# Kernel optimization log

Hardware: AMD Instinct MI355X
Metric: run time of the kernel (lower is better)

The kernel has to match this reference:

```python
import jax, jax.numpy as jnp
import numpy as np

N_HEADS = 8
D_MODEL = 512
D_HEAD = 64
INIT_RANGE = 0.02
B = 2
T = 192
IGNORE = -1000000.0


def setup_inputs() -> dict:
    key = jax.random.key(0)
    ks = jax.random.split(key, 10)
    def p(k, shape):
        return jax.random.normal(k, shape, dtype=jnp.float32) * INIT_RANGE
    inp = {
        "normalized_resid_pre": jax.random.normal(ks[0], (B, T, D_MODEL), dtype=jnp.float32),
        "W_A": p(ks[1], (N_HEADS, D_MODEL, D_HEAD)),
        "W_B": p(ks[2], (N_HEADS, D_MODEL, D_HEAD)),
        "W_C": p(ks[3], (N_HEADS, D_MODEL, D_HEAD)),
        "W_D": p(ks[4], (N_HEADS, D_MODEL, D_HEAD)),
        "W_E": p(ks[5], (N_HEADS, D_MODEL, D_HEAD)),
        "W_K": p(ks[6], (N_HEADS, D_HEAD, D_HEAD, D_HEAD)),
        "W_V": p(ks[7], (N_HEADS, D_HEAD, D_HEAD, D_HEAD)),
        "W_O": p(ks[8], (N_HEADS, D_HEAD, D_MODEL)),
        "b_A": jnp.zeros((N_HEADS, D_HEAD), jnp.float32),
        "b_B": jnp.zeros((N_HEADS, D_HEAD), jnp.float32),
        "b_C": jnp.zeros((N_HEADS, D_HEAD), jnp.float32),
        "b_D": jnp.zeros((N_HEADS, D_HEAD), jnp.float32),
        "b_E": jnp.zeros((N_HEADS, D_HEAD), jnp.float32),
        "b_O": jnp.zeros((D_MODEL,), jnp.float32),
    }
    return inp


def reference(normalized_resid_pre, W_A, W_B, W_C, W_D, W_E, W_K, W_V, W_O,
              b_A, b_B, b_C, b_D, b_E, b_O):
    x = normalized_resid_pre
    bs, ts, _ = x.shape
    # Per-head linear projections: [b, p, n, h]
    a = jnp.einsum('ndh,bpd->bpnh', W_A, x) + b_A
    b = jnp.einsum('ndh,bpd->bpnh', W_B, x) + b_B
    c = jnp.einsum('ndh,bpd->bpnh', W_C, x) + b_C
    d = jnp.einsum('ndh,bpd->bpnh', W_D, x) + b_D
    e = jnp.einsum('ndh,bpd->bpnh', W_E, x) + b_E
    # Pairwise value tensor: v[b, p1, p2, n, h3]
    v = jnp.einsum('bpnh,bqng,nhgk->bpqnk', d, e, W_V)
    # Cubic key contraction. NOTE: step2 sums over heads of b (faithful to original einsum).
    step1 = jnp.einsum('brnk,nijk->brij', c, W_K)        # [b, p3, i, j]
    step2 = jnp.einsum('brij,bqnj->briq', step1, b)      # [b, p3, i, p2]
    scores = jnp.einsum('briq,bpni->bnpqr', step2, a)    # [b, n, p1, p2, p3]
    # Causal mask (order_attn=True): mask where p1 >= p2 or p1 >= p3
    i1 = jnp.arange(ts)[:, None, None]
    i2 = jnp.arange(ts)[None, :, None]
    i3 = jnp.arange(ts)[None, None, :]
    mask = (i1 >= i2) | (i1 >= i3)
    scores = jnp.where(mask, IGNORE, scores)
    # [b, n, p3, p1*p2], scaled by d_head
    scores = scores.transpose(0, 1, 4, 2, 3).reshape(bs, N_HEADS, ts, ts * ts) / D_HEAD
    extra = jnp.full((bs, N_HEADS, ts, 1), -1000.0, scores.dtype)
    probs = jax.nn.softmax(jnp.concatenate([scores, extra], axis=-1), axis=-1)
    # v -> [b, n, h, p1*p2], append zero slot matching the extra score column
    vflat = v.transpose(0, 3, 4, 1, 2).reshape(bs, N_HEADS, D_HEAD, ts * ts)
    vflat = jnp.concatenate([vflat, jnp.zeros((bs, N_HEADS, D_HEAD, 1), vflat.dtype)], axis=-1)
    z = jnp.einsum('bnql,bnhl->bqnh', probs, vflat)
    out = jnp.einsum('bpnh,nhd->bpd', z, W_O) + b_O
    return out
```

## Files before the change

### kernel.cpp

```cpp
#include <hip/hip_runtime.h>
#include <hip/hip_bf16.h>
#include <math.h>


#define OFF_A      0u
#define OFF_Bp     196608u
#define OFF_C      393216u
#define OFF_D      589824u
#define OFF_E      786432u
#define OFF_BSUM   983040u
#define OFF_S1     1007616u
#define OFF_S2     2580480u
#define OFF_Z      7299072u

typedef short s8v __attribute__((ext_vector_type(8)));
typedef float f4v __attribute__((ext_vector_type(4)));

static __device__ __forceinline__ unsigned short f2bf(float f) {
  union { float f; unsigned int u; } v; v.f = f;
  unsigned int r = v.u + 0x7FFFu + ((v.u >> 16) & 1u);
  return (unsigned short)(r >> 16);
}


__device__ __forceinline__ void load_At(const float* __restrict__ Aptr, int lda,
                                        float* __restrict__ As, int t) {
  int r = t >> 2, c4 = (t & 3) * 4;
  const float4 v = *(const float4*)(Aptr + r * lda + c4);
  As[(c4 + 0) * 68 + r] = v.x;
  As[(c4 + 1) * 68 + r] = v.y;
  As[(c4 + 2) * 68 + r] = v.z;
  As[(c4 + 3) * 68 + r] = v.w;
}

__device__ __forceinline__ void mm_acc16(const float* __restrict__ As,
                                         const float* __restrict__ Bs,
                                         float acc[4][4], int tm4, int tn4) {
#pragma unroll
  for (int kk = 0; kk < 16; ++kk) {
    const float4 a = *(const float4*)(As + kk * 68 + tm4);
    const float4 b = *(const float4*)(Bs + kk * 68 + tn4);
    acc[0][0] += a.x * b.x; acc[0][1] += a.x * b.y; acc[0][2] += a.x * b.z; acc[0][3] += a.x * b.w;
    acc[1][0] += a.y * b.x; acc[1][1] += a.y * b.y; acc[1][2] += a.y * b.z; acc[1][3] += a.y * b.w;
    acc[2][0] += a.z * b.x; acc[2][1] += a.z * b.y; acc[2][2] += a.z * b.z; acc[2][3] += a.z * b.w;
    acc[3][0] += a.w * b.x; acc[3][1] += a.w * b.y; acc[3][2] += a.w * b.z; acc[3][3] += a.w * b.w;
  }
}


__global__ void k_proj(const float* __restrict__ x,
                       const float* __restrict__ W0, const float* __restrict__ W1,
                       const float* __restrict__ W2, const float* __restrict__ W3,
                       const float* __restrict__ W4,
                       const float* __restrict__ bi0, const float* __restrict__ bi1,
                       const float* __restrict__ bi2, const float* __restrict__ bi3,
                       const float* __restrict__ bi4,
                       float* __restrict__ ws) {
  const int wsel = blockIdx.z;
  const float* W = wsel == 0 ? W0 : wsel == 1 ? W1 : wsel == 2 ? W2 : wsel == 3 ? W3 : W4;
  const float* bias = wsel == 0 ? bi0 : wsel == 1 ? bi1 : wsel == 2 ? bi2 : wsel == 3 ? bi3 : bi4;
  float* out = ws + (size_t)wsel * 196608u;

  const int m0 = blockIdx.x * 64;
  const int c0 = blockIdx.y * 64;
  const int nblk = c0 >> 6;
  __shared__ float As[16 * 68], Bs[16 * 68];
  const int t = threadIdx.x;
  const int tm4 = (t >> 4) * 4, tn4 = (t & 15) * 4;
  float acc[4][4] = {};

  for (int k0 = 0; k0 < 512; k0 += 16) {
    load_At(x + m0 * 512 + k0, 512, As, t);
#pragma unroll
    for (int it = 0; it < 4; ++it) {
      int kk = (t >> 6) + it * 4, cc = t & 63;
      Bs[kk * 68 + cc] = W[nblk * 32768 + (k0 + kk) * 64 + cc];
    }
    __syncthreads();
    mm_acc16(As, Bs, acc, tm4, tn4);
    __syncthreads();
  }
  const float4 bv = *(const float4*)&bias[c0 + tn4];
#pragma unroll
  for (int i = 0; i < 4; ++i) {
    float4 v;
    v.x = acc[i][0] + bv.x; v.y = acc[i][1] + bv.y; v.z = acc[i][2] + bv.z; v.w = acc[i][3] + bv.w;
    *(float4*)&out[(m0 + tm4 + i) * 512 + c0 + tn4] = v;
  }
}


__global__ void k_bsum(const float* __restrict__ bp, float* __restrict__ out) {
  int idx = blockIdx.x * 256 + threadIdx.x;
  if (idx < 24576) {
    int bq = idx >> 6, j = idx & 63;
    float s = 0.f;
#pragma unroll
    for (int n = 0; n < 8; ++n) s += bp[bq * 512 + n * 64 + j];
    out[idx] = s;
  }
}


__global__ void k_step1(const float* __restrict__ Cp, const float* __restrict__ WK,
                        float* __restrict__ S1) {
  const int m0 = blockIdx.x * 64, c0 = blockIdx.y * 64;
  __shared__ float As[16 * 68], Bs[16 * 68];
  const int t = threadIdx.x;
  const int tm4 = (t >> 4) * 4, tn4 = (t & 15) * 4;
  float acc[4][4] = {};
  for (int k0 = 0; k0 < 512; k0 += 16) {
    load_At(Cp + m0 * 512 + k0, 512, As, t);
#pragma unroll
    for (int it = 0; it < 4; ++it) {
      int kk = t & 15, cc = (t >> 4) + it * 16;
      int k = k0 + kk;
      Bs[kk * 68 + cc] = WK[(k >> 6) * 262144 + (c0 + cc) * 64 + (k & 63)];
    }
    __syncthreads();
    mm_acc16(As, Bs, acc, tm4, tn4);
    __syncthreads();
  }
#pragma unroll
  for (int i = 0; i < 4; ++i) {
    float4 v; v.x = acc[i][0]; v.y = acc[i][1]; v.z = acc[i][2]; v.w = acc[i][3];
    *(float4*)&S1[(size_t)(m0 + tm4 + i) * 4096 + c0 + tn4] = v;
  }
}


__global__ void k_step2(const float* __restrict__ S1, const float* __restrict__ BS,
                        float* __restrict__ S2) {
  const int b = blockIdx.z;
  const int m0 = blockIdx.x * 64, c0 = blockIdx.y * 64;
  const float* A = S1 + (size_t)b * 786432u;
  const float* Bb = BS + b * 12288;
  float* C = S2 + (size_t)b * 2359296u;
  __shared__ float As[16 * 68], Bs[16 * 68];
  const int t = threadIdx.x;
  const int tm4 = (t >> 4) * 4, tn4 = (t & 15) * 4;
  float acc[4][4] = {};
  for (int k0 = 0; k0 < 64; k0 += 16) {
    load_At(A + m0 * 64 + k0, 64, As, t);
#pragma unroll
    for (int it = 0; it < 4; ++it) {
      int kk = t & 15, cc = (t >> 4) + it * 16;
      Bs[kk * 68 + cc] = Bb[(c0 + cc) * 64 + k0 + kk];
    }
    __syncthreads();
    mm_acc16(As, Bs, acc, tm4, tn4);
    __syncthreads();
  }
#pragma unroll
  for (int i = 0; i < 4; ++i) {
    float4 v; v.x = acc[i][0]; v.y = acc[i][1]; v.z = acc[i][2]; v.w = acc[i][3];
    *(float4*)&C[(size_t)(m0 + tm4 + i) * 192 + c0 + tn4] = v;
  }
}

#define X_ST2T 0u
#define X_ET   27648u
#define X_E    53248u
#define X_AS   78848u
#define X_DT   88064u
#define X_FT   97280u
#define X_RED  106496u
#define X_TOT  108544u
#define X_US   0u
#define X_RZ   27648u

extern "C" __global__ void __launch_bounds__(512, 1)
k_attn(const float* __restrict__ st2, const float* __restrict__ eproj,
       const float* __restrict__ aproj, const float* __restrict__ dproj,
       const float* __restrict__ WV, float* __restrict__ zout) {
  extern __shared__ char smc[];
  unsigned short* lus = (unsigned short*)smc;
  float* lf = (float*)smc;
  const int bn = blockIdx.x;
  const int r = 191 - (int)blockIdx.y;
  const int b = bn >> 3, n = bn & 7;
  const int t = threadIdx.x;
  const int lane = t & 63, w = t >> 6;
  const int l15 = lane & 15, kg = lane >> 4;

  const float* st2g = st2 + (size_t)b * 2359296u + (size_t)r * 12288u;
  const float* eg = eproj + (size_t)b * 98304u + n * 64;
  const float* ag = aproj + (size_t)b * 98304u + n * 64;
  const float* dg = dproj + (size_t)b * 98304u + n * 64;

  for (int idx = t; idx < 12288; idx += 512) {
    int i = idx / 192, q = idx - i * 192;
    lus[(X_ST2T >> 1) + q * 72 + i] = f2bf(st2g[idx]);
  }
  for (int idx = t; idx < 12288; idx += 512) {
    int q = idx >> 6, g = idx & 63;
    lus[(X_ET >> 1) + g * 200 + q] = f2bf(eg[q * 512 + g]);
  }

  float Dpart = 0.f;
  f4v U0 = {0.f, 0.f, 0.f, 0.f};
  f4v U1 = {0.f, 0.f, 0.f, 0.f};
  const int ptiles = (r + 63) >> 6;

  for (int pt_i = 0; pt_i < ptiles; ++pt_i) {
    const int p0 = pt_i << 6;
    for (int idx = t; idx < 4096; idx += 512) {
      int p = idx >> 6, c = idx & 63;
      float av = ag[(p0 + p) * 512 + c];
      float dv = dg[(p0 + p) * 512 + c];
      lus[(X_AS >> 1) + p * 72 + c] = f2bf(av);
      lus[(X_DT >> 1) + c * 72 + p] = f2bf(dv);
    }
    __syncthreads();

#pragma unroll
    for (int s = 0; s < 6; ++s) {
      const int tid = w + 8 * s, qt = tid >> 2, pt = tid & 3;
      f4v acc = {0.f, 0.f, 0.f, 0.f};
#pragma unroll
      for (int kb = 0; kb < 2; ++kb) {
        const s8v A = *(const s8v*)&lus[(X_ST2T >> 1) + (qt * 16 + l15) * 72 + kb * 32 + kg * 8];
        const s8v Bf = *(const s8v*)&lus[(X_AS >> 1) + (pt * 16 + l15) * 72 + kb * 32 + kg * 8];
        acc = __builtin_amdgcn_mfma_f32_16x16x32_bf16(A, Bf, acc, 0, 0, 0);
      }
      const int p_loc = pt * 16 + l15, p = p0 + p_loc;
      short4 pk;
      {
        float Ev0 = 0.f, Ev1 = 0.f, Ev2 = 0.f, Ev3 = 0.f;
        const int q0 = qt * 16 + kg * 4;
        if (p < r) {
          if (q0 + 0 > p) { Ev0 = __expf(acc[0] * 0.015625f); Dpart += Ev0; }
          if (q0 + 1 > p) { Ev1 = __expf(acc[1] * 0.015625f); Dpart += Ev1; }
          if (q0 + 2 > p) { Ev2 = __expf(acc[2] * 0.015625f); Dpart += Ev2; }
          if (q0 + 3 > p) { Ev3 = __expf(acc[3] * 0.015625f); Dpart += Ev3; }
        }
        pk.x = (short)f2bf(Ev0); pk.y = (short)f2bf(Ev1);
        pk.z = (short)f2bf(Ev2); pk.w = (short)f2bf(Ev3);
      }
      *(short4*)&lus[(X_E >> 1) + p_loc * 200 + qt * 16 + kg * 4] = pk;
    }
    __syncthreads();

#pragma unroll
    for (int s = 0; s < 2; ++s) {
      const int tid = w + 8 * s, mt = tid >> 2, nt = tid & 3;
      f4v acc = {0.f, 0.f, 0.f, 0.f};
#pragma unroll
      for (int kb = 0; kb < 6; ++kb) {
        const s8v A = *(const s8v*)&lus[(X_E >> 1) + (mt * 16 + l15) * 200 + kb * 32 + kg * 8];
        const s8v Bf = *(const s8v*)&lus[(X_ET >> 1) + (nt * 16 + l15) * 200 + kb * 32 + kg * 8];
        acc = __builtin_amdgcn_mfma_f32_16x16x32_bf16(A, Bf, acc, 0, 0, 0);
      }
      short4 pk;
      pk.x = (short)f2bf(acc[0]); pk.y = (short)f2bf(acc[1]);
      pk.z = (short)f2bf(acc[2]); pk.w = (short)f2bf(acc[3]);
      *(short4*)&lus[(X_FT >> 1) + (nt * 16 + l15) * 72 + mt * 16 + kg * 4] = pk;
    }
    __syncthreads();

    {
      const int tid0 = w, ht0 = tid0 >> 2, gt0 = tid0 & 3;
#pragma unroll
      for (int kb = 0; kb < 2; ++kb) {
        const s8v A = *(const s8v*)&lus[(X_DT >> 1) + (ht0 * 16 + l15) * 72 + kb * 32 + kg * 8];
        const s8v Bf = *(const s8v*)&lus[(X_FT >> 1) + (gt0 * 16 + l15) * 72 + kb * 32 + kg * 8];
        U0 = __builtin_amdgcn_mfma_f32_16x16x32_bf16(A, Bf, U0, 0, 0, 0);
      }
      const int tid1 = w + 8, ht1 = tid1 >> 2, gt1 = tid1 & 3;
#pragma unroll
      for (int kb = 0; kb < 2; ++kb) {
        const s8v A = *(const s8v*)&lus[(X_DT >> 1) + (ht1 * 16 + l15) * 72 + kb * 32 + kg * 8];
        const s8v Bf = *(const s8v*)&lus[(X_FT >> 1) + (gt1 * 16 + l15) * 72 + kb * 32 + kg * 8];
        U1 = __builtin_amdgcn_mfma_f32_16x16x32_bf16(A, Bf, U1, 0, 0, 0);
      }
    }
    __syncthreads();
  }

  lf[(X_RED >> 2) + t] = Dpart;
  __syncthreads();
  for (int off = 256; off > 0; off >>= 1) {
    if (t < off) lf[(X_RED >> 2) + t] += lf[(X_RED >> 2) + t + off];
    __syncthreads();
  }
  const float Dfull = lf[X_RED >> 2];
  const float invD = Dfull > 0.f ? 1.f / Dfull : 0.f;
  __syncthreads();

  {
    const int ht0 = w >> 2, gt0 = w & 3;
#pragma unroll
    for (int j = 0; j < 4; ++j)
      lf[(X_US >> 2) + (gt0 * 16 + l15) * 66 + ht0 * 16 + kg * 4 + j] = U0[j] * invD;
    const int ht1 = (w + 8) >> 2, gt1 = (w + 8) & 3;
#pragma unroll
    for (int j = 0; j < 4; ++j)
      lf[(X_US >> 2) + (gt1 * 16 + l15) * 66 + ht1 * 16 + kg * 4 + j] = U1[j] * invD;
  }
  __syncthreads();

  const float* WVn = WV + (size_t)n * 262144u;
  const int k4 = (t & 15) * 4, hh = t >> 4;
  float zx = 0.f, zy = 0.f, zz = 0.f, zw = 0.f;
#pragma unroll
  for (int hi = 0; hi < 2; ++hi) {
    const int h = hh * 2 + hi;
    const float* wr = WVn + (size_t)h * 4096 + k4;
    for (int g = 0; g < 64; ++g) {
      const float u = lf[(X_US >> 2) + g * 66 + h];
      const float4 wv = *(const float4*)(wr + g * 64);
      zx += u * wv.x; zy += u * wv.y; zz += u * wv.z; zw += u * wv.w;
    }
  }
  { float4 zp; zp.x = zx; zp.y = zy; zp.z = zz; zp.w = zw;
    *(float4*)&lf[(X_RZ >> 2) + hh * 64 + k4] = zp; }
  __syncthreads();
  if (t < 64) {
    float z = 0.f;
#pragma unroll 8
    for (int c = 0; c < 32; ++c) z += lf[(X_RZ >> 2) + c * 64 + t];
    zout[(size_t)(b * 192 + r) * 512 + n * 64 + t] = z;
  }
}


__global__ void k_out(const float* __restrict__ Z, const float* __restrict__ WO,
                      const float* __restrict__ bO, float* __restrict__ out) {
  const int m0 = blockIdx.x * 64, c0 = blockIdx.y * 64;
  __shared__ float As[16 * 68], Bs[16 * 68];
  const int t = threadIdx.x;
  const int tm4 = (t >> 4) * 4, tn4 = (t & 15) * 4;
  float acc[4][4] = {};
  for (int k0 = 0; k0 < 512; k0 += 16) {
    load_At(Z + m0 * 512 + k0, 512, As, t);
#pragma unroll
    for (int it = 0; it < 4; ++it) {
      int kk = (t >> 6) + it * 4, cc = t & 63;
      Bs[kk * 68 + cc] = WO[(k0 + kk) * 512 + c0 + cc];
    }
    __syncthreads();
    mm_acc16(As, Bs, acc, tm4, tn4);
    __syncthreads();
  }
  const float4 bv = *(const float4*)&bO[c0 + tn4];
#pragma unroll
  for (int i = 0; i < 4; ++i) {
    float4 v;
    v.x = acc[i][0] + bv.x; v.y = acc[i][1] + bv.y; v.z = acc[i][2] + bv.z; v.w = acc[i][3] + bv.w;
    *(float4*)&out[(m0 + tm4 + i) * 512 + c0 + tn4] = v;
  }
}


extern "C" void kernel_launch(void* const* d_in, const int* in_sizes, int n_in,
                              void* d_out, int out_size, void* d_ws, size_t ws_size,
                              hipStream_t stream) {
  const float* x  = (const float*)d_in[0];
  const float* WA = (const float*)d_in[1];
  const float* WB = (const float*)d_in[2];
  const float* WC = (const float*)d_in[3];
  const float* WD = (const float*)d_in[4];
  const float* WE = (const float*)d_in[5];
  const float* WK = (const float*)d_in[6];
  const float* WV = (const float*)d_in[7];
  const float* WO = (const float*)d_in[8];
  const float* bA = (const float*)d_in[9];
  const float* bB = (const float*)d_in[10];
  const float* bC = (const float*)d_in[11];
  const float* bD = (const float*)d_in[12];
  const float* bE = (const float*)d_in[13];
  const float* bO = (const float*)d_in[14];
  float* ws = (float*)d_ws;
  float* out = (float*)d_out;

  dim3 blk(256);
  k_proj<<<dim3(6, 8, 5), blk, 0, stream>>>(x, WA, WB, WC, WD, WE, bA, bB, bC, bD, bE, ws);
  k_bsum<<<dim3(96), blk, 0, stream>>>(ws + OFF_Bp, ws + OFF_BSUM);
  k_step1<<<dim3(6, 64), blk, 0, stream>>>(ws + OFF_C, WK, ws + OFF_S1);
  k_step2<<<dim3(192, 3, 2), blk, 0, stream>>>(ws + OFF_S1, ws + OFF_BSUM, ws + OFF_S2);

  hipFuncSetAttribute((const void*)k_attn, hipFuncAttributeMaxDynamicSharedMemorySize, X_TOT);
  k_attn<<<dim3(16, 192), dim3(512), X_TOT, stream>>>(ws + OFF_S2, ws + OFF_E, ws + OFF_A,
                                                      ws + OFF_D, WV, ws + OFF_Z);

  k_out<<<dim3(6, 8), blk, 0, stream>>>(ws + OFF_Z, WO, bO, out);
}
```

Measured before the change: 440.9 us.

## Tile attention over q blocks, cut LDS footprint, raise occupancy bound

Splits the q dimension of the score/exp tile into 64-wide blocks processed inside the p-tile loop. Each block streams its E slice and accumulates F = E·Eᵀ in registers across q tiles, so the full 192-wide E and Eᵀ buffers are no longer held in LDS. It also skips q tiles entirely below the causal diagonal. The smaller LDS footprint lets launch bounds allow more blocks per CU for better occupancy, at the cost of extra barriers and repeated global loads of E per p tile.

```diff
diff --git a/kernel.cpp b/kernel.cpp
--- a/kernel.cpp
+++ b/kernel.cpp
@@ -159,17 +159,17 @@
 }
 
 #define X_ST2T 0u
-#define X_ET   27648u
-#define X_E    53248u
-#define X_AS   78848u
-#define X_DT   88064u
-#define X_FT   97280u
-#define X_RED  106496u
-#define X_TOT  108544u
+#define X_AS   27648u
+#define X_DT   36864u
+#define X_FT   46080u
+#define X_ET   55296u
+#define X_E    64512u
+#define X_RED  73728u
+#define X_TOT  75776u
 #define X_US   0u
 #define X_RZ   27648u
 
-extern "C" __global__ void __launch_bounds__(512, 1)
+extern "C" __global__ void __launch_bounds__(512, 4)
 k_attn(const float* __restrict__ st2, const float* __restrict__ eproj,
        const float* __restrict__ aproj, const float* __restrict__ dproj,
        const float* __restrict__ WV, float* __restrict__ zout) {
@@ -192,10 +192,6 @@
     int i = idx / 192, q = idx - i * 192;
     lus[(X_ST2T >> 1) + q * 72 + i] = f2bf(st2g[idx]);
   }
-  for (int idx = t; idx < 12288; idx += 512) {
-    int q = idx >> 6, g = idx & 63;
-    lus[(X_ET >> 1) + g * 200 + q] = f2bf(eg[q * 512 + g]);
-  }
 
   float Dpart = 0.f;
   f4v U0 = {0.f, 0.f, 0.f, 0.f};
@@ -206,67 +202,90 @@
     const int p0 = pt_i << 6;
     for (int idx = t; idx < 4096; idx += 512) {
       int p = idx >> 6, c = idx & 63;
-      float av = ag[(p0 + p) * 512 + c];
-      float dv = dg[(p0 + p) * 512 + c];
-      lus[(X_AS >> 1) + p * 72 + c] = f2bf(av);
-      lus[(X_DT >> 1) + c * 72 + p] = f2bf(dv);
-    }
-    __syncthreads();
-
-#pragma unroll
-    for (int s = 0; s < 6; ++s) {
-      const int tid = w + 8 * s, qt = tid >> 2, pt = tid & 3;
-      f4v acc = {0.f, 0.f, 0.f, 0.f};
-#pragma unroll
-      for (int kb = 0; kb < 2; ++kb) {
-        const s8v A = *(const s8v*)&lus[(X_ST2T >> 1) + (qt * 16 + l15) * 72 + kb * 32 + kg * 8];
-        const s8v Bf = *(const s8v*)&lus[(X_AS >> 1) + (pt * 16 + l15) * 72 + kb * 32 + kg * 8];
-        acc = __builtin_amdgcn_mfma_f32_16x16x32_bf16(A, Bf, acc, 0, 0, 0);
+      lus[(X_AS >> 1) + p * 72 + c] = f2bf(ag[(p0 + p) * 512 + c]);
+      lus[(X_DT >> 1) + c * 72 + p] = f2bf(dg[(p0 + p) * 512 + c]);
+    }
+
+    f4v F0 = {0.f, 0.f, 0.f, 0.f};
+    f4v F1 = {0.f, 0.f, 0.f, 0.f};
+
+    for (int qt = pt_i; qt < 3; ++qt) {
+      const int q0 = qt << 6;
+      for (int idx = t; idx < 4096; idx += 512) {
+        int ql = idx >> 6, g = idx & 63;
+        lus[(X_ET >> 1) + g * 72 + ql] = f2bf(eg[(q0 + ql) * 512 + g]);
       }
-      const int p_loc = pt * 16 + l15, p = p0 + p_loc;
-      short4 pk;
-      {
+      __syncthreads();
+
+#pragma unroll
+      for (int s = 0; s < 2; ++s) {
+        const int tid = w + 8 * s, qt2 = tid >> 2, pt2 = tid & 3;
+        f4v acc = {0.f, 0.f, 0.f, 0.f};
+#pragma unroll
+        for (int kb = 0; kb < 2; ++kb) {
+          const s8v A = *(const s8v*)&lus[(X_ST2T >> 1) + (q0 + qt2 * 16 + l15) * 72 + kb * 32 + kg * 8];
+          const s8v Bf = *(const s8v*)&lus[(X_AS >> 1) + (pt2 * 16 + l15) * 72 + kb * 32 + kg * 8];
+          acc = __builtin_amdgcn_mfma_f32_16x16x32_bf16(A, Bf, acc, 0, 0, 0);
+        }
+        const int p_loc = pt2 * 16 + l15, p = p0 + p_loc;
+        const int ql0 = qt2 * 16 + kg * 4;
         float Ev0 = 0.f, Ev1 = 0.f, Ev2 = 0.f, Ev3 = 0.f;
-        const int q0 = qt * 16 + kg * 4;
         if (p < r) {
-          if (q0 + 0 > p) { Ev0 = __expf(acc[0] * 0.015625f); Dpart += Ev0; }
-          if (q0 + 1 > p) { Ev1 = __expf(acc[1] * 0.015625f); Dpart += Ev1; }
-          if (q0 + 2 > p) { Ev2 = __expf(acc[2] * 0.015625f); Dpart += Ev2; }
-          if (q0 + 3 > p) { Ev3 = __expf(acc[3] * 0.015625f); Dpart += Ev3; }
+          const int q = q0 + ql0;
+          if (q + 0 > p) { Ev0 = __expf(acc[0] * 0.015625f); Dpart += Ev0; }
+          if (q + 1 > p) { Ev1 = __expf(acc[1] * 0.015625f); Dpart += Ev1; }
+          if (q + 2 > p) { Ev2 = __expf(acc[2] * 0.015625f); Dpart += Ev2; }
+          if (q + 3 > p) { Ev3 = __expf(acc[3] * 0.015625f); Dpart += Ev3; }
         }
+        short4 pk;
         pk.x = (short)f2bf(Ev0); pk.y = (short)f2bf(Ev1);
         pk.z = (short)f2bf(Ev2); pk.w = (short)f2bf(Ev3);
+        *(short4*)&lus[(X_E >> 1) + p_loc * 72 + ql0] = pk;
       }
-      *(short4*)&lus[(X_E >> 1) + p_loc * 200 + qt * 16 + kg * 4] = pk;
-    }
-    __syncthreads();
-
-#pragma unroll
-    for (int s = 0; s < 2; ++s) {
-      const int tid = w + 8 * s, mt = tid >> 2, nt = tid & 3;
-      f4v acc = {0.f, 0.f, 0.f, 0.f};
-#pragma unroll
-      for (int kb = 0; kb < 6; ++kb) {
-        const s8v A = *(const s8v*)&lus[(X_E >> 1) + (mt * 16 + l15) * 200 + kb * 32 + kg * 8];
-        const s8v Bf = *(const s8v*)&lus[(X_ET >> 1) + (nt * 16 + l15) * 200 + kb * 32 + kg * 8];
-        acc = __builtin_amdgcn_mfma_f32_16x16x32_bf16(A, Bf, acc, 0, 0, 0);
+      __syncthreads();
+
+      {
+        const int mt0 = w >> 2, nt0 = w & 3;
+#pragma unroll
+        for (int kb = 0; kb < 2; ++kb) {
+          const s8v A = *(const s8v*)&lus[(X_E >> 1) + (mt0 * 16 + l15) * 72 + kb * 32 + kg * 8];
+          const s8v Bf = *(const s8v*)&lus[(X_ET >> 1) + (nt0 * 16 + l15) * 72 + kb * 32 + kg * 8];
+          F0 = __builtin_amdgcn_mfma_f32_16x16x32_bf16(A, Bf, F0, 0, 0, 0);
+        }
+        const int mt1 = (w + 8) >> 2, nt1 = (w + 8) & 3;
+#pragma unroll
+        for (int kb = 0; kb < 2; ++kb) {
+          const s8v A = *(const s8v*)&lus[(X_E >> 1) + (mt1 * 16 + l15) * 72 + kb * 32 + kg * 8];
+          const s8v Bf = *(const s8v*)&lus[(X_ET >> 1) + (nt1 * 16 + l15) * 72 + kb * 32 + kg * 8];
+          F1 = __builtin_amdgcn_mfma_f32_16x16x32_bf16(A, Bf, F1, 0, 0, 0);
+        }
       }
-      short4 pk;
-      pk.x = (short)f2bf(acc[0]); pk.y = (short)f2bf(acc[1]);
-      pk.z = (short)f2bf(acc[2]); pk.w = (short)f2bf(acc[3]);
-      *(short4*)&lus[(X_FT >> 1) + (nt * 16 + l15) * 72 + mt * 16 + kg * 4] = pk;
-    }
-    __syncthreads();
+      __syncthreads();
+    }
 
     {
-      const int tid0 = w, ht0 = tid0 >> 2, gt0 = tid0 & 3;
+      const int mt0 = w >> 2, nt0 = w & 3;
+      short4 pk0;
+      pk0.x = (short)f2bf(F0[0]); pk0.y = (short)f2bf(F0[1]);
+      pk0.z = (short)f2bf(F0[2]); pk0.w = (short)f2bf(F0[3]);
+      *(short4*)&lus[(X_FT >> 1) + (nt0 * 16 + l15) * 72 + mt0 * 16 + kg * 4] = pk0;
+      const int mt1 = (w + 8) >> 2, nt1 = (w + 8) & 3;
+      short4 pk1;
+      pk1.x = (short)f2bf(F1[0]); pk1.y = (short)f2bf(F1[1]);
+      pk1.z = (short)f2bf(F1[2]); pk1.w = (short)f2bf(F1[3]);
+      *(short4*)&lus[(X_FT >> 1) + (nt1 * 16 + l15) * 72 + mt1 * 16 + kg * 4] = pk1;
+    }
+    __syncthreads();
+
+    {
+      const int ht0 = w >> 2, gt0 = w & 3;
 #pragma unroll
       for (int kb = 0; kb < 2; ++kb) {
         const s8v A = *(const s8v*)&lus[(X_DT >> 1) + (ht0 * 16 + l15) * 72 + kb * 32 + kg * 8];
         const s8v Bf = *(const s8v*)&lus[(X_FT >> 1) + (gt0 * 16 + l15) * 72 + kb * 32 + kg * 8];
         U0 = __builtin_amdgcn_mfma_f32_16x16x32_bf16(A, Bf, U0, 0, 0, 0);
       }
-      const int tid1 = w + 8, ht1 = tid1 >> 2, gt1 = tid1 & 3;
+      const int ht1 = (w + 8) >> 2, gt1 = (w + 8) & 3;
 #pragma unroll
       for (int kb = 0; kb < 2; ++kb) {
         const s8v A = *(const s8v*)&lus[(X_DT >> 1) + (ht1 * 16 + l15) * 72 + kb * 32 + kg * 8];
```

New measurement: 481.9 us. +9.3%, slower.
